# Kernel tuning notes

Hardware: AMD Instinct MI355X
Metric: run time of the kernel (lower is better)

Reference implementation:

```python
import jax, jax.numpy as jnp
import numpy as np

DIM = 768
NUM_HEADS = 12
HEAD_DIM = DIM // NUM_HEADS  # 64
HH = 48
WW = 48
REL_LEN = 2 * HH - 1  # 95
THETA = 10000.0


def _rope_freqs(dim, end_x, end_y, theta=THETA):
    # matches _compute_rope_frequencies: (end_x*end_y, dim//2) cos/sin tables
    freqs = 1.0 / theta ** (jnp.arange(0, dim, 4)[: dim // 4].astype(jnp.float32) / dim)
    t = jnp.arange(end_x * end_y, dtype=jnp.float32)
    t_x = t % end_x
    t_y = jnp.floor(t / end_x)
    f = jnp.concatenate([t_x[:, None] * freqs[None, :], t_y[:, None] * freqs[None, :]], axis=-1)
    return jnp.cos(f), jnp.sin(f)


def _rel_bias(size, rel_pos):
    # q_size == k_size == size, rel_pos already has length 2*size-1 -> pure gather
    coords = jnp.arange(size)[:, None] - jnp.arange(size)[None, :] + (size - 1)
    return rel_pos[coords]  # (size, size, C)


def setup_inputs() -> dict:
    key = jax.random.key(0)
    ks = jax.random.split(key, 6)
    x = jax.random.normal(ks[0], (1, HH, WW, DIM), dtype=jnp.float32)
    w_qkv = jax.random.normal(ks[1], (DIM, 3 * DIM), dtype=jnp.float32) * 0.02
    b_qkv = jnp.zeros((3 * DIM,), dtype=jnp.float32)
    w_proj = jax.random.normal(ks[2], (DIM, DIM), dtype=jnp.float32) * 0.02
    b_proj = jnp.zeros((DIM,), dtype=jnp.float32)
    rel_pos_h = jax.random.normal(ks[3], (REL_LEN, HEAD_DIM), dtype=jnp.float32) * 0.02
    rel_pos_w = jax.random.normal(ks[4], (REL_LEN, HEAD_DIM), dtype=jnp.float32) * 0.02
    return {"x": x, "w_qkv": w_qkv, "b_qkv": b_qkv, "w_proj": w_proj,
            "b_proj": b_proj, "rel_pos_h": rel_pos_h, "rel_pos_w": rel_pos_w}


def reference(x, w_qkv, b_qkv, w_proj, b_proj, rel_pos_h, rel_pos_w):
    B, H, W, dim = x.shape
    L = H * W
    nh, hd = NUM_HEADS, dim // NUM_HEADS
    scale = hd ** (-0.5)

    qkv = (x.reshape(B, L, dim) @ w_qkv + b_qkv).reshape(B, L, 3, nh, hd)
    qkv = qkv.transpose(2, 0, 3, 1, 4)  # (3, B, nh, L, hd)
    q, k, v = qkv[0], qkv[1], qkv[2]

    # inline RoPE (real-valued, pairwise rotation)
    cosf, sinf = _rope_freqs(hd, W, H)  # (L, hd//2)
    c = cosf[None, None]  # (1,1,L,hd//2)
    s = sinf[None, None]

    def rot(t):
        tr = t.reshape(B, nh, L, hd // 2, 2)
        t0, t1 = tr[..., 0], tr[..., 1]
        return jnp.stack([t0 * c - t1 * s, t0 * s + t1 * c], axis=-1).reshape(B, nh, L, hd)

    q = rot(q)
    k = rot(k)

    attn = jnp.einsum('bnqd,bnkd->bnqk', q, k) * scale  # (B, nh, L, L)

    # decomposed relative position bias
    bias_h = _rel_bias(H, rel_pos_h)  # (H, H, hd)
    bias_w = _rel_bias(W, rel_pos_w)  # (W, W, hd)
    q6 = q.reshape(B, nh, H, W, hd)
    rel_h = jnp.einsum('bnhwc,hkc->bnhwk', q6, bias_h)  # (B,nh,H,W,Hk)
    rel_w = jnp.einsum('bnhwc,wkc->bnhwk', q6, bias_w)  # (B,nh,H,W,Wk)
    attn = (attn.reshape(B, nh, H, W, H, W)
            + rel_h[..., :, None]   # broadcast over key-W
            + rel_w[..., None, :])  # broadcast over key-H
    attn = attn.reshape(B, nh, L, L)

    attn = jax.nn.softmax(attn, axis=-1)
    out = jnp.einsum('bnqk,bnkd->bnqd', attn, v)  # (B, nh, L, hd)
    out = out.transpose(0, 2, 1, 3).reshape(B, H, W, dim)
    return out @ w_proj + b_proj
```

## Files before the change

kernel.cpp:

```cpp
#include <hip/hip_runtime.h>
#include <hip/hip_bf16.h>


typedef short bf16x8 __attribute__((ext_vector_type(8)));
typedef float f32x4  __attribute__((ext_vector_type(4)));
typedef _Float16 f16x4 __attribute__((ext_vector_type(4)));

namespace {
constexpr int LTOK = 2304;
constexpr int DIMC = 768;
constexpr int NH   = 12;
constexpr int HD   = 64;
constexpr int WG   = 48;
constexpr int QKVN = 2304;
constexpr int EXT2 = 128;
constexpr int NSPLIT = 3;
constexpr int KPS  = LTOK / NSPLIT;
constexpr int NT   = KPS / 64;
constexpr int NQB2 = LTOK / 128;
constexpr float SCALE = 0.125f;
constexpr int NB_ROPE = (LTOK * 32) / 256;
constexpr int NB_CAST = (LTOK * DIMC / 8) / 256;
constexpr int NB_TQKV = (QKVN / 32) * (DIMC / 32);
constexpr int NB_TPRJ = (DIMC / 32) * (DIMC / 32);
}

__device__ __forceinline__ short f2b(float f) {
    __hip_bfloat16 h = __float2bfloat16(f);
    return *reinterpret_cast<short*>(&h);
}
__device__ __forceinline__ float b2f(short s) {
    return __uint_as_float(((unsigned)(unsigned short)s) << 16);
}
__device__ __forceinline__ void load16_to_lds(const short* g, short* l) {
    __builtin_amdgcn_global_load_lds(
        (__attribute__((address_space(1))) void*)g,
        (__attribute__((address_space(3))) void*)l,
        16, 0, 0);
}
__device__ __forceinline__ f16x4 nt_load_h4(const _Float16* p) {
    return __builtin_nontemporal_load((const f16x4*)p);
}

__global__ __launch_bounds__(256) void prep_kernel(
    const float* __restrict__ x, const float* __restrict__ w_qkv,
    const float* __restrict__ w_proj,
    float* __restrict__ cost, float* __restrict__ sint,
    short* __restrict__ xb, short* __restrict__ wqkvT, short* __restrict__ wprojT)
{
    __shared__ float ts[32][36];
    const int b = blockIdx.x;
    const int t = threadIdx.x;
    if (b < NB_ROPE) {
        int idx = b * 256 + t;
        int j = idx & 31;
        int l = idx >> 5;
        float tt = (j < 16) ? (float)(l % WG) : (float)(l / WG);
        int fi = j & 15;
        float freq = powf(10000.0f, -(float)fi / 16.0f);
        float ang = tt * freq;
        cost[idx] = cosf(ang);
        sint[idx] = sinf(ang);
    } else if (b < NB_ROPE + NB_CAST) {
        int i = (b - NB_ROPE) * 256 + t;
        float4 a = ((const float4*)x)[2 * i];
        float4 bb = ((const float4*)x)[2 * i + 1];
        bf16x8 o;
        o[0] = f2b(a.x); o[1] = f2b(a.y); o[2] = f2b(a.z); o[3] = f2b(a.w);
        o[4] = f2b(bb.x); o[5] = f2b(bb.y); o[6] = f2b(bb.z); o[7] = f2b(bb.w);
        ((bf16x8*)xb)[i] = o;
    } else {
        const float* in;
        short* out;
        int R, C, c0, r0;
        if (b < NB_ROPE + NB_CAST + NB_TQKV) {
            int flat = b - NB_ROPE - NB_CAST;
            in = w_qkv; out = wqkvT; R = DIMC; C = QKVN;
            c0 = (flat % (QKVN / 32)) * 32;
            r0 = (flat / (QKVN / 32)) * 32;
        } else {
            int flat = b - NB_ROPE - NB_CAST - NB_TQKV;
            in = w_proj; out = wprojT; R = DIMC; C = DIMC;
            c0 = (flat % (DIMC / 32)) * 32;
            r0 = (flat / (DIMC / 32)) * 32;
        }
        {
            int r = t >> 3, cb = (t & 7) * 4;
            float4 v = *(const float4*)&in[(size_t)(r0 + r) * C + c0 + cb];
            ts[r][cb] = v.x; ts[r][cb + 1] = v.y; ts[r][cb + 2] = v.z; ts[r][cb + 3] = v.w;
        }
        __syncthreads();
        {
            int oc = t >> 3, rb = (t & 7) * 4;
            short4 s;
            s.x = f2b(ts[rb][oc]);     s.y = f2b(ts[rb + 1][oc]);
            s.z = f2b(ts[rb + 2][oc]); s.w = f2b(ts[rb + 3][oc]);
            *(short4*)&out[(size_t)(c0 + oc) * R + r0 + rb] = s;
        }
    }
}

__global__ __launch_bounds__(256) void gemm_bf16_64x128_kernel(
    const short* __restrict__ A, const short* __restrict__ Bt,
    const float* __restrict__ bias, float* __restrict__ C,
    int M, int N, int K)
{
    __shared__ short As[64 * 64];
    __shared__ short Bs[128 * 64];
    const int tid = threadIdx.x;
    const int bm = blockIdx.y * 64, bn = blockIdx.x * 128;
    const int w = tid >> 6, l = tid & 63;
    const int lm = l & 15, lk = (l >> 4) * 8;

    f32x4 acc[4][2];
    const f32x4 zf = {0.f, 0.f, 0.f, 0.f};
    #pragma unroll
    for (int m = 0; m < 4; ++m)
        #pragma unroll
        for (int n = 0; n < 2; ++n) acc[m][n] = zf;

    for (int k0 = 0; k0 < K; k0 += 64) {
        __syncthreads();
        #pragma unroll
        for (int p = 0; p < 2; ++p) {
            int f = tid + p * 256;
            int row = f >> 3, c8 = (f & 7) * 8;
            load16_to_lds(&A[(size_t)(bm + row) * K + k0 + c8], &As[f * 8]);
        }
        #pragma unroll
        for (int p = 0; p < 4; ++p) {
            int f = tid + p * 256;
            int row = f >> 3, c8 = (f & 7) * 8;
            load16_to_lds(&Bt[(size_t)(bn + row) * K + k0 + c8], &Bs[f * 8]);
        }
        __syncthreads();
        #pragma unroll
        for (int kh = 0; kh < 2; ++kh) {
            bf16x8 a[4], b[2];
            #pragma unroll
            for (int m = 0; m < 4; ++m)
                a[m] = *(const bf16x8*)&As[(m * 16 + lm) * 64 + kh * 32 + lk];
            #pragma unroll
            for (int n = 0; n < 2; ++n)
                b[n] = *(const bf16x8*)&Bs[(w * 32 + n * 16 + lm) * 64 + kh * 32 + lk];
            #pragma unroll
            for (int m = 0; m < 4; ++m)
                #pragma unroll
                for (int n = 0; n < 2; ++n)
                    acc[m][n] = __builtin_amdgcn_mfma_f32_16x16x32_bf16(a[m], b[n], acc[m][n], 0, 0, 0);
        }
    }
    const int orow = (l >> 4) * 4;
    #pragma unroll
    for (int m = 0; m < 4; ++m) {
        #pragma unroll
        for (int n = 0; n < 2; ++n) {
            int col = bn + w * 32 + n * 16 + lm;
            float bv = bias[col];
            #pragma unroll
            for (int r = 0; r < 4; ++r) {
                int row = bm + m * 16 + orow + r;
                C[(size_t)row * N + col] = acc[m][n][r] + bv;
            }
        }
    }
}

__global__ __launch_bounds__(512) void gemm64_512_kernel(
    const short* __restrict__ A, const short* __restrict__ Bt,
    const float* __restrict__ bias, float* __restrict__ C,
    int M, int N, int K)
{
    __shared__ short As[64 * 64];
    __shared__ short Bs[64 * 64];
    const int tid = threadIdx.x;
    const int bm = blockIdx.y * 64, bn = blockIdx.x * 64;
    const int w = tid >> 6, l = tid & 63;
    const int wr = w >> 2;
    const int wc = w & 3;
    const int lm = l & 15, lk = (l >> 4) * 8;

    f32x4 acc[2][1];
    const f32x4 zf = {0.f, 0.f, 0.f, 0.f};
    acc[0][0] = zf; acc[1][0] = zf;

    for (int k0 = 0; k0 < K; k0 += 64) {
        __syncthreads();
        {
            int f = tid;
            int row = f >> 3, c8 = (f & 7) * 8;
            load16_to_lds(&A[(size_t)(bm + row) * K + k0 + c8], &As[f * 8]);
            load16_to_lds(&Bt[(size_t)(bn + row) * K + k0 + c8], &Bs[f * 8]);
        }
        __syncthreads();
        #pragma unroll
        for (int kh = 0; kh < 2; ++kh) {
            bf16x8 a[2], b;
            #pragma unroll
            for (int m = 0; m < 2; ++m)
                a[m] = *(const bf16x8*)&As[(wr * 32 + m * 16 + lm) * 64 + kh * 32 + lk];
            b = *(const bf16x8*)&Bs[(wc * 16 + lm) * 64 + kh * 32 + lk];
            #pragma unroll
            for (int m = 0; m < 2; ++m)
                acc[m][0] = __builtin_amdgcn_mfma_f32_16x16x32_bf16(a[m], b, acc[m][0], 0, 0, 0);
        }
    }
    const int orow = (l >> 4) * 4;
    #pragma unroll
    for (int m = 0; m < 2; ++m) {
        int col = bn + wc * 16 + lm;
        float bv = bias[col];
        #pragma unroll
        for (int r = 0; r < 4; ++r) {
            int row = bm + wr * 32 + m * 16 + orow + r;
            C[(size_t)row * N + col] = acc[m][0][r] + bv;
        }
    }
}

__global__ __launch_bounds__(256) void split_rope_relbias_kernel(
    const float* __restrict__ qkv_raw,
    const float* __restrict__ cost, const float* __restrict__ sint,
    const float* __restrict__ rel_pos_h, const float* __restrict__ rel_pos_w,
    short* __restrict__ q_ext, short* __restrict__ kb, short* __restrict__ vT,
    short* __restrict__ relh_g)
{
    __shared__ short vt_s[64][72];
    __shared__ float qf32[64][68];
    __shared__ float rph_st[49][68];
    __shared__ float rpw_st[95][68];
    __shared__ short outw[64][64];
    __shared__ short outh[64][48];

    const int h = blockIdx.y;
    const int l0 = blockIdx.x * 64;
    const int hmin = l0 / WG;
    const int t = threadIdx.x;
    const int tok = t >> 2, dq = (t & 3) * 16;
    const int l = l0 + tok;
    const float* row = qkv_raw + (size_t)l * QKVN + h * HD;

    bf16x8 qe[2], kv[2];
    #pragma unroll
    for (int i = 0; i < 16; i += 4) {
        int d = dq + i;
        float4 tq = *(const float4*)&row[d];
        float4 tk = *(const float4*)&row[DIMC + d];
        float4 tv = *(const float4*)&row[2 * DIMC + d];
        float2 c01 = *(const float2*)&cost[l * 32 + d / 2];
        float2 s01 = *(const float2*)&sint[l * 32 + d / 2];
        float q0 = tq.x * c01.x - tq.y * s01.x;
        float q1 = tq.x * s01.x + tq.y * c01.x;
        float q2 = tq.z * c01.y - tq.w * s01.y;
        float q3 = tq.z * s01.y + tq.w * c01.y;
        qe[i >> 3][(i & 7) + 0] = f2b(q0 * SCALE);
        qe[i >> 3][(i & 7) + 1] = f2b(q1 * SCALE);
        qe[i >> 3][(i & 7) + 2] = f2b(q2 * SCALE);
        qe[i >> 3][(i & 7) + 3] = f2b(q3 * SCALE);
        kv[i >> 3][(i & 7) + 0] = f2b(tk.x * c01.x - tk.y * s01.x);
        kv[i >> 3][(i & 7) + 1] = f2b(tk.x * s01.x + tk.y * c01.x);
        kv[i >> 3][(i & 7) + 2] = f2b(tk.z * c01.y - tk.w * s01.y);
        kv[i >> 3][(i & 7) + 3] = f2b(tk.z * s01.y + tk.w * c01.y);
        vt_s[d + 0][tok] = f2b(tv.x);
        vt_s[d + 1][tok] = f2b(tv.y);
        vt_s[d + 2][tok] = f2b(tv.z);
        vt_s[d + 3][tok] = f2b(tv.w);
    }
    size_t kbase = ((size_t)h * LTOK + l) * HD + dq;
    *(bf16x8*)&kb[kbase]     = kv[0];
    *(bf16x8*)&kb[kbase + 8] = kv[1];
    size_t ebase = ((size_t)h * LTOK + l) * EXT2 + dq;
    *(bf16x8*)&q_ext[ebase]     = qe[0];
    *(bf16x8*)&q_ext[ebase + 8] = qe[1];
    #pragma unroll
    for (int i = 0; i < 8; ++i) {
        qf32[tok][dq + i]     = b2f(qe[0][i]);
        qf32[tok][dq + 8 + i] = b2f(qe[1][i]);
    }
    {
        const bf16x8 z8 = {0, 0, 0, 0, 0, 0, 0, 0};
        ((bf16x8*)outw)[t] = z8;
        ((bf16x8*)outw)[t + 256] = z8;
    }
    __syncthreads();
    {
        const int drow = t >> 2, lq = (t & 3) * 16;
        bf16x8 v0 = *(bf16x8*)&vt_s[drow][lq];
        bf16x8 v1 = *(bf16x8*)&vt_s[drow][lq + 8];
        size_t vbase = ((size_t)h * HD + drow) * LTOK + l0 + lq;
        *(bf16x8*)&vT[vbase]     = v0;
        *(bf16x8*)&vT[vbase + 8] = v1;
    }
    for (int i = t; i < (49 + 95) * 16; i += 256) {
        int rr = i >> 4, c4 = (i & 15) * 4;
        if (rr < 49)
            *(float4*)&rph_st[rr][c4] = *(const float4*)&rel_pos_h[(size_t)(hmin + rr) * HD + c4];
        else
            *(float4*)&rpw_st[rr - 49][c4] = *(const float4*)&rel_pos_w[(size_t)(rr - 49) * HD + c4];
    }
    __syncthreads();
    {
        const int ti = t >> 2, sub = t & 3;
        const int ll = l0 + ti;
        const int hh = ll / WG, ww = ll % WG;
        const int hoff = hh - hmin;
        for (int ko = sub; ko < 96; ko += 4) {
            bool ish = ko < 48;
            int kk = ish ? ko : ko - 48;
            const float* br = ish ? &rph_st[hoff + 47 - kk][0] : &rpw_st[ww + 47 - kk][0];
            float s = 0.f;
            #pragma unroll
            for (int c = 0; c < HD; c += 4) {
                float4 a = *(const float4*)&qf32[ti][c];
                float4 b = *(const float4*)&br[c];
                s += a.x * b.x + a.y * b.y + a.z * b.z + a.w * b.w;
            }
            s *= 8.0f;
            if (ish) outh[ti][kk] = f2b(s);
            else     outw[ti][2 + kk] = f2b(s);
        }
    }
    __syncthreads();
    #pragma unroll
    for (int p = 0; p < 2; ++p) {
        int i = t + p * 256;
        int r2 = i >> 3, c8 = (i & 7) * 8;
        *(bf16x8*)&q_ext[((size_t)h * LTOK + l0 + r2) * EXT2 + 64 + c8] =
            *(const bf16x8*)&outw[r2][c8];
    }
    for (int i = t; i < 384; i += 256) {
        int r2 = i / 6, c8 = (i % 6) * 8;
        *(bf16x8*)&relh_g[((size_t)h * LTOK + l0 + r2) * WG + c8] =
            *(const bf16x8*)&outh[r2][c8];
    }
}

__global__ __launch_bounds__(256, 3) void attn_kernel(
    const short* __restrict__ q_ext, const short* __restrict__ kb,
    const short* __restrict__ vT, const short* __restrict__ relh_g,
    _Float16* __restrict__ o_part, float* __restrict__ lsum_g)
{
    __shared__ short ks[64][136];
    __shared__ short vs[64][72];
    __shared__ short rh[128][56];

    const int qblk = blockIdx.x;
    const int n = blockIdx.y;
    const int sp = blockIdx.z;
    const int q0 = qblk * 128;
    const int key_base = sp * KPS;
    const int tid = threadIdx.x;
    const int w = tid >> 6, l = tid & 63;
    const int lm = l & 15, g = l >> 4;
    const int lk = g * 8;

    const short* qeh = q_ext + (size_t)n * LTOK * EXT2;
    const short* kh  = kb + (size_t)n * LTOK * HD;
    const short* vh  = vT + (size_t)n * HD * LTOK;

    bf16x8 qf[2][4];
    #pragma unroll
    for (int t = 0; t < 2; ++t)
        #pragma unroll
        for (int kk = 0; kk < 4; ++kk)
            qf[t][kk] = *(const bf16x8*)&qeh[(size_t)(q0 + w * 32 + t * 16 + lm) * EXT2 + kk * 32 + lk];

    for (int i = tid; i < 128 * 6; i += 256) {
        int row = i / 6, c8 = (i % 6) * 8;
        *(bf16x8*)&rh[row][c8] =
            *(const bf16x8*)&relh_g[((size_t)n * LTOK + q0 + row) * WG + c8];
    }
    {
        const bf16x8 z8 = {0, 0, 0, 0, 0, 0, 0, 0};
        #pragma unroll
        for (int p = 0; p < 2; ++p) {
            int i = tid + p * 256;
            int row = i >> 3, c8 = (i & 7) * 8;
            *(bf16x8*)&ks[row][64 + c8] = z8;
        }
    }
    const short ONE = f2b(1.0f);
    int kap = 0, prev_wi = 66;
    if (tid < 64) {
        int f_ = tid >> 4, m_ = tid & 15;
        kap = 32 * (f_ >> 1) + 8 * (m_ >> 2) + 4 * (f_ & 1) + (m_ & 3);
        prev_wi = 66 + (key_base + kap) % WG;
    }

    bf16x8 kreg[2], vreg[2];
    #define ISSUE_LOADS(kt_)  do {                                              \
        const int key0_ = key_base + (kt_) * 64;                                \
        _Pragma("unroll")                                                       \
        for (int p = 0; p < 2; ++p) {                                           \
            int fl_ = tid + p * 256;                                            \
            int rho_ = fl_ >> 3, c8_ = (fl_ & 7) * 8;                           \
            int f_ = rho_ >> 4, m_ = rho_ & 15;                                 \
            int kap_ = 32 * (f_ >> 1) + 8 * (m_ >> 2) + 4 * (f_ & 1) + (m_ & 3);\
            kreg[p] = *(const bf16x8*)&kh[(size_t)(key0_ + kap_) * HD + c8_];   \
        }                                                                       \
        _Pragma("unroll")                                                       \
        for (int p = 0; p < 2; ++p) {                                           \
            int fl_ = tid + p * 256;                                            \
            int row_ = fl_ >> 3, c8_ = (fl_ & 7) * 8;                           \
            vreg[p] = *(const bf16x8*)&vh[(size_t)row_ * LTOK + key0_ + c8_];   \
        }                                                                       \
    } while (0)

    float lsum[2] = {0.f, 0.f};
    f32x4 oacc[2][4];
    const f32x4 zf = {0.f, 0.f, 0.f, 0.f};
    #pragma unroll
    for (int t = 0; t < 2; ++t)
        #pragma unroll
        for (int d = 0; d < 4; ++d) oacc[t][d] = zf;

    ISSUE_LOADS(0);

    for (int kt = 0; kt < NT; ++kt) {
        const int key0 = key_base + kt * 64;
        const int A = key0 / WG;
        const int T = WG * (A + 1);
        __syncthreads();
        #pragma unroll
        for (int p = 0; p < 2; ++p) {
            int fl = tid + p * 256;
            int rho = fl >> 3, c8 = (fl & 7) * 8;
            *(bf16x8*)&ks[rho][c8] = kreg[p];
        }
        #pragma unroll
        for (int p = 0; p < 2; ++p) {
            int fl = tid + p * 256;
            int row = fl >> 3, c8 = (fl & 7) * 8;
            *(bf16x8*)&vs[row][c8] = vreg[p];
        }
        if (tid < 64) {
            int key = key0 + kap;
            ks[tid][64] = (key < T) ? ONE : (short)0;
            ks[tid][65] = (key < T) ? (short)0 : ONE;
            ks[tid][prev_wi] = 0;
            int wcol = 66 + key % WG;
            ks[tid][wcol] = ONE;
            prev_wi = wcol;
        }
        if (kt + 1 < NT) { ISSUE_LOADS(kt + 1); }
        __builtin_amdgcn_sched_barrier(0);
        __syncthreads();

        if (g == 0) {
            #pragma unroll
            for (int t = 0; t < 2; ++t) {
                int row = w * 32 + t * 16 + lm;
                qf[t][2][0] = rh[row][A];
                qf[t][2][1] = rh[row][A + 1];
            }
        }

        f32x4 st[2][4];
        #pragma unroll
        for (int t = 0; t < 2; ++t)
            #pragma unroll
            for (int f = 0; f < 4; ++f) st[t][f] = zf;
        __builtin_amdgcn_s_setprio(1);
        #pragma unroll
        for (int f = 0; f < 4; ++f)
            #pragma unroll
            for (int kk = 0; kk < 4; ++kk) {
                bf16x8 kf = *(const bf16x8*)&ks[f * 16 + lm][kk * 32 + lk];
                st[0][f] = __builtin_amdgcn_mfma_f32_16x16x32_bf16(kf, qf[0][kk], st[0][f], 0, 0, 0);
                st[1][f] = __builtin_amdgcn_mfma_f32_16x16x32_bf16(kf, qf[1][kk], st[1][f], 0, 0, 0);
            }
        __builtin_amdgcn_s_setprio(0);
        bf16x8 pf[2][2];
        #pragma unroll
        for (int t = 0; t < 2; ++t)
            #pragma unroll
            for (int f = 0; f < 4; ++f)
                #pragma unroll
                for (int r = 0; r < 4; ++r) {
                    float p = __expf(st[t][f][r]);
                    lsum[t] += p;
                    pf[t][f >> 1][(f & 1) * 4 + r] = f2b(p);
                }
        __builtin_amdgcn_s_setprio(1);
        #pragma unroll
        for (int kk = 0; kk < 2; ++kk)
            #pragma unroll
            for (int d = 0; d < 4; ++d) {
                bf16x8 vf = *(const bf16x8*)&vs[d * 16 + lm][kk * 32 + lk];
                oacc[0][d] = __builtin_amdgcn_mfma_f32_16x16x32_bf16(pf[0][kk], vf, oacc[0][d], 0, 0, 0);
                oacc[1][d] = __builtin_amdgcn_mfma_f32_16x16x32_bf16(pf[1][kk], vf, oacc[1][d], 0, 0, 0);
            }
        __builtin_amdgcn_s_setprio(0);
    }
    #undef ISSUE_LOADS

    size_t pbase = (((size_t)n * NQB2 + qblk) * NSPLIT + sp) * (128 * 64);
    #pragma unroll
    for (int t = 0; t < 2; ++t)
        #pragma unroll
        for (int d = 0; d < 4; ++d) {
            f16x4 hv;
            #pragma unroll
            for (int r = 0; r < 4; ++r) hv[r] = (_Float16)oacc[t][d][r];
            __builtin_nontemporal_store(hv,
                (f16x4*)&o_part[pbase + (size_t)(((w * 2 + t) * 4 + d) * 256) + l * 4]);
        }
    size_t lb = (((size_t)n * NQB2 + qblk) * NSPLIT + sp) * 128;
    #pragma unroll
    for (int t = 0; t < 2; ++t) {
        float s = lsum[t];
        s += __shfl_xor(s, 16);
        s += __shfl_xor(s, 32);
        if (l < 16) lsum_g[lb + w * 32 + t * 16 + l] = s;
    }
}

__global__ __launch_bounds__(256) void combine_kernel(
    const _Float16* __restrict__ o_part, const float* __restrict__ lsum_g,
    short* __restrict__ o)
{
    __shared__ short ost[128][72];
    const int qblk = blockIdx.x, h = blockIdx.y;
    const int tid = threadIdx.x;
    const int w = tid >> 6, l = tid & 63;
    const int lm = l & 15, g = l >> 4;
    size_t sb = ((size_t)h * NQB2 + qblk) * NSPLIT;

    float inv[2][4];
    #pragma unroll
    for (int t = 0; t < 2; ++t)
        #pragma unroll
        for (int r = 0; r < 4; ++r) {
            int row = w * 32 + t * 16 + g * 4 + r;
            float ls = 0.f;
            #pragma unroll
            for (int s = 0; s < NSPLIT; ++s)
                ls += lsum_g[(sb + s) * 128 + row];
            inv[t][r] = 1.0f / ls;
        }
    #pragma unroll
    for (int t = 0; t < 2; ++t)
        #pragma unroll
        for (int d = 0; d < 4; ++d) {
            size_t off = (size_t)(((w * 2 + t) * 4 + d) * 256) + l * 4;
            float acc[4] = {0.f, 0.f, 0.f, 0.f};
            #pragma unroll
            for (int s = 0; s < NSPLIT; ++s) {
                f16x4 hv = nt_load_h4(&o_part[(sb + s) * 8192 + off]);
                #pragma unroll
                for (int r = 0; r < 4; ++r) acc[r] += (float)hv[r];
            }
            #pragma unroll
            for (int r = 0; r < 4; ++r)
                ost[w * 32 + t * 16 + g * 4 + r][d * 16 + lm] = f2b(acc[r] * inv[t][r]);
        }
    __syncthreads();
    const int row = tid >> 1, cb = (tid & 1) * 32;
    size_t ob = ((size_t)(qblk * 128 + row)) * DIMC + h * 64 + cb;
    #pragma unroll
    for (int v = 0; v < 4; ++v)
        *(bf16x8*)&o[ob + v * 8] = *(const bf16x8*)&ost[row][cb + v * 8];
}

extern "C" void kernel_launch(void* const* d_in, const int* in_sizes, int n_in,
                              void* d_out, int out_size, void* d_ws, size_t ws_size,
                              hipStream_t stream) {
    (void)in_sizes; (void)n_in; (void)out_size; (void)ws_size;
    const float* x         = (const float*)d_in[0];
    const float* w_qkv     = (const float*)d_in[1];
    const float* b_qkv     = (const float*)d_in[2];
    const float* w_proj    = (const float*)d_in[3];
    const float* b_proj    = (const float*)d_in[4];
    const float* rel_pos_h = (const float*)d_in[5];
    const float* rel_pos_w = (const float*)d_in[6];
    float* out = (float*)d_out;

    float* qkv_raw   = (float*)d_ws;
    short* xb        = (short*)(qkv_raw + (size_t)LTOK * QKVN);
    short* wqkvT     = xb + (size_t)LTOK * DIMC;
    float* cost      = (float*)(wqkvT + (size_t)QKVN * DIMC);
    float* sint      = cost + (size_t)LTOK * 32;
    _Float16* o_part = (_Float16*)qkv_raw;
    short* wprojT  = (short*)(sint + (size_t)LTOK * 32);
    short* q_ext   = wprojT + (size_t)DIMC * DIMC;
    short* kb      = q_ext + (size_t)NH * LTOK * EXT2;
    short* vTb     = kb + (size_t)NH * LTOK * HD;
    short* ob      = vTb + (size_t)NH * LTOK * HD;
    short* relh_g  = ob + (size_t)LTOK * DIMC;
    float* lsum_g  = (float*)(relh_g + (size_t)NH * LTOK * WG);

    prep_kernel<<<dim3(NB_ROPE + NB_CAST + NB_TQKV + NB_TPRJ), 256, 0, stream>>>(
        x, w_qkv, w_proj, cost, sint, xb, wqkvT, wprojT);

    gemm_bf16_64x128_kernel<<<dim3(QKVN / 128, LTOK / 64), 256, 0, stream>>>(
        xb, wqkvT, b_qkv, qkv_raw, LTOK, QKVN, DIMC);

    split_rope_relbias_kernel<<<dim3(LTOK / 64, NH), 256, 0, stream>>>(
        qkv_raw, cost, sint, rel_pos_h, rel_pos_w, q_ext, kb, vTb, relh_g);

    attn_kernel<<<dim3(NQB2, NH, NSPLIT), 256, 0, stream>>>(
        q_ext, kb, vTb, relh_g, o_part, lsum_g);

    combine_kernel<<<dim3(NQB2, NH), 256, 0, stream>>>(o_part, lsum_g, ob);

    gemm64_512_kernel<<<dim3(DIMC / 64, LTOK / 64), 512, 0, stream>>>(
        ob, wprojT, b_proj, out, LTOK, DIMC, DIMC);
}
```

Measured before the change: 97.30 us.

## Use 2-wave attention blocks with 64 query rows per wave; retile proj GEMM to 32x64

The attention kernel now runs 128 threads (2 waves) per block, and each wave handles 64 query rows instead of 32. Each K/V fragment read from LDS therefore feeds twice as many MFMAs, and the score computation is processed one key fragment at a time to limit live registers. The output projection GEMM moves from 64x64 tiles with 512 threads to 32x64 tiles with 256 threads, doubling the block count. The cost is higher register pressure in the attention kernel (larger oacc and qf arrays), fewer waves per CU for hiding latency, and more global-load work per thread.

Measured after the change: 116.1 us. 19.3% more time.

```diff
diff --git a/kernel.cpp b/kernel.cpp
--- a/kernel.cpp
+++ b/kernel.cpp
@@ -166,30 +166,32 @@
     }
 }
 
-__global__ __launch_bounds__(512) void gemm64_512_kernel(
+__global__ __launch_bounds__(256) void gemm32x64_kernel(
     const short* __restrict__ A, const short* __restrict__ Bt,
     const float* __restrict__ bias, float* __restrict__ C,
     int M, int N, int K)
 {
-    __shared__ short As[64 * 64];
+    __shared__ short As[32 * 64];
     __shared__ short Bs[64 * 64];
     const int tid = threadIdx.x;
-    const int bm = blockIdx.y * 64, bn = blockIdx.x * 64;
+    const int bm = blockIdx.y * 32, bn = blockIdx.x * 64;
     const int w = tid >> 6, l = tid & 63;
-    const int wr = w >> 2;
-    const int wc = w & 3;
     const int lm = l & 15, lk = (l >> 4) * 8;
 
-    f32x4 acc[2][1];
+    f32x4 acc[2];
     const f32x4 zf = {0.f, 0.f, 0.f, 0.f};
-    acc[0][0] = zf; acc[1][0] = zf;
+    acc[0] = zf; acc[1] = zf;
 
     for (int k0 = 0; k0 < K; k0 += 64) {
         __syncthreads();
         {
-            int f = tid;
+            int row = tid >> 3, c8 = (tid & 7) * 8;
+            load16_to_lds(&A[(size_t)(bm + row) * K + k0 + c8], &As[tid * 8]);
+        }
+        #pragma unroll
+        for (int p = 0; p < 2; ++p) {
+            int f = tid + p * 256;
             int row = f >> 3, c8 = (f & 7) * 8;
-            load16_to_lds(&A[(size_t)(bm + row) * K + k0 + c8], &As[f * 8]);
             load16_to_lds(&Bt[(size_t)(bn + row) * K + k0 + c8], &Bs[f * 8]);
         }
         __syncthreads();
@@ -198,22 +200,22 @@
             bf16x8 a[2], b;
             #pragma unroll
             for (int m = 0; m < 2; ++m)
-                a[m] = *(const bf16x8*)&As[(wr * 32 + m * 16 + lm) * 64 + kh * 32 + lk];
-            b = *(const bf16x8*)&Bs[(wc * 16 + lm) * 64 + kh * 32 + lk];
+                a[m] = *(const bf16x8*)&As[(m * 16 + lm) * 64 + kh * 32 + lk];
+            b = *(const bf16x8*)&Bs[(w * 16 + lm) * 64 + kh * 32 + lk];
             #pragma unroll
             for (int m = 0; m < 2; ++m)
-                acc[m][0] = __builtin_amdgcn_mfma_f32_16x16x32_bf16(a[m], b, acc[m][0], 0, 0, 0);
+                acc[m] = __builtin_amdgcn_mfma_f32_16x16x32_bf16(a[m], b, acc[m], 0, 0, 0);
         }
     }
     const int orow = (l >> 4) * 4;
     #pragma unroll
     for (int m = 0; m < 2; ++m) {
-        int col = bn + wc * 16 + lm;
+        int col = bn + w * 16 + lm;
         float bv = bias[col];
         #pragma unroll
         for (int r = 0; r < 4; ++r) {
-            int row = bm + wr * 32 + m * 16 + orow + r;
-            C[(size_t)row * N + col] = acc[m][0][r] + bv;
+            int row = bm + m * 16 + orow + r;
+            C[(size_t)row * N + col] = acc[m][r] + bv;
         }
     }
 }
@@ -335,7 +337,7 @@
     }
 }
 
-__global__ __launch_bounds__(256, 3) void attn_kernel(
+__global__ __launch_bounds__(128, 2) void attn_kernel(
     const short* __restrict__ q_ext, const short* __restrict__ kb,
     const short* __restrict__ vT, const short* __restrict__ relh_g,
     _Float16* __restrict__ o_part, float* __restrict__ lsum_g)
@@ -358,14 +360,14 @@
     const short* kh  = kb + (size_t)n * LTOK * HD;
     const short* vh  = vT + (size_t)n * HD * LTOK;
 
-    bf16x8 qf[2][4];
-    #pragma unroll
-    for (int t = 0; t < 2; ++t)
+    bf16x8 qf[4][4];
+    #pragma unroll
+    for (int t = 0; t < 4; ++t)
         #pragma unroll
         for (int kk = 0; kk < 4; ++kk)
-            qf[t][kk] = *(const bf16x8*)&qeh[(size_t)(q0 + w * 32 + t * 16 + lm) * EXT2 + kk * 32 + lk];
-
-    for (int i = tid; i < 128 * 6; i += 256) {
+            qf[t][kk] = *(const bf16x8*)&qeh[(size_t)(q0 + w * 64 + t * 16 + lm) * EXT2 + kk * 32 + lk];
+
+    for (int i = tid; i < 128 * 6; i += 128) {
         int row = i / 6, c8 = (i % 6) * 8;
         *(bf16x8*)&rh[row][c8] =
             *(const bf16x8*)&relh_g[((size_t)n * LTOK + q0 + row) * WG + c8];
@@ -373,8 +375,8 @@
     {
         const bf16x8 z8 = {0, 0, 0, 0, 0, 0, 0, 0};
         #pragma unroll
-        for (int p = 0; p < 2; ++p) {
-            int i = tid + p * 256;
+        for (int p = 0; p < 4; ++p) {
+            int i = tid + p * 128;
             int row = i >> 3, c8 = (i & 7) * 8;
             *(bf16x8*)&ks[row][64 + c8] = z8;
         }
@@ -387,30 +389,30 @@
         prev_wi = 66 + (key_base + kap) % WG;
     }
 
-    bf16x8 kreg[2], vreg[2];
+    bf16x8 kreg[4], vreg[4];
     #define ISSUE_LOADS(kt_)  do {                                              \
         const int key0_ = key_base + (kt_) * 64;                                \
         _Pragma("unroll")                                                       \
-        for (int p = 0; p < 2; ++p) {                                           \
-            int fl_ = tid + p * 256;                                            \
+        for (int p = 0; p < 4; ++p) {                                           \
+            int fl_ = tid + p * 128;                                            \
             int rho_ = fl_ >> 3, c8_ = (fl_ & 7) * 8;                           \
             int f_ = rho_ >> 4, m_ = rho_ & 15;                                 \
             int kap_ = 32 * (f_ >> 1) + 8 * (m_ >> 2) + 4 * (f_ & 1) + (m_ & 3);\
             kreg[p] = *(const bf16x8*)&kh[(size_t)(key0_ + kap_) * HD + c8_];   \
         }                                                                       \
         _Pragma("unroll")                                                       \
-        for (int p = 0; p < 2; ++p) {                                           \
-            int fl_ = tid + p * 256;                                            \
+        for (int p = 0; p < 4; ++p) {                                           \
+            int fl_ = tid + p * 128;                                            \
             int row_ = fl_ >> 3, c8_ = (fl_ & 7) * 8;                           \
             vreg[p] = *(const bf16x8*)&vh[(size_t)row_ * LTOK + key0_ + c8_];   \
         }                                                                       \
     } while (0)
 
-    float lsum[2] = {0.f, 0.f};
-    f32x4 oacc[2][4];
+    float lsum[4] = {0.f, 0.f, 0.f, 0.f};
+    f32x4 oacc[4][4];
     const f32x4 zf = {0.f, 0.f, 0.f, 0.f};
     #pragma unroll
-    for (int t = 0; t < 2; ++t)
+    for (int t = 0; t < 4; ++t)
         #pragma unroll
         for (int d = 0; d < 4; ++d) oacc[t][d] = zf;
 
@@ -422,14 +424,14 @@
         const int T = WG * (A + 1);
         __syncthreads();
         #pragma unroll
-        for (int p = 0; p < 2; ++p) {
-            int fl = tid + p * 256;
+        for (int p = 0; p < 4; ++p) {
+            int fl = tid + p * 128;
             int rho = fl >> 3, c8 = (fl & 7) * 8;
             *(bf16x8*)&ks[rho][c8] = kreg[p];
         }
         #pragma unroll
-        for (int p = 0; p < 2; ++p) {
-            int fl = tid + p * 256;
+        for (int p = 0; p < 4; ++p) {
+            int fl = tid + p * 128;
             int row = fl >> 3, c8 = (fl & 7) * 8;
             *(bf16x8*)&vs[row][c8] = vreg[p];
         }
@@ -448,47 +450,46 @@
 
         if (g == 0) {
             #pragma unroll
-            for (int t = 0; t < 2; ++t) {
-                int row = w * 32 + t * 16 + lm;
+            for (int t = 0; t < 4; ++t) {
+                int row = w * 64 + t * 16 + lm;
                 qf[t][2][0] = rh[row][A];
                 qf[t][2][1] = rh[row][A + 1];
             }
         }
 
-        f32x4 st[2][4];
-        #pragma unroll
-        for (int t = 0; t < 2; ++t)
-            #pragma unroll
-            for (int f = 0; f < 4; ++f) st[t][f] = zf;
-        __builtin_amdgcn_s_setprio(1);
-        #pragma unroll
-        for (int f = 0; f < 4; ++f)
+        bf16x8 pf[4][2];
+        #pragma unroll
+        for (int f = 0; f < 4; ++f) {
+            f32x4 stf[4];
+            #pragma unroll
+            for (int t = 0; t < 4; ++t) stf[t] = zf;
+            __builtin_amdgcn_s_setprio(1);
             #pragma unroll
             for (int kk = 0; kk < 4; ++kk) {
                 bf16x8 kf = *(const bf16x8*)&ks[f * 16 + lm][kk * 32 + lk];
-                st[0][f] = __builtin_amdgcn_mfma_f32_16x16x32_bf16(kf, qf[0][kk], st[0][f], 0, 0, 0);
-                st[1][f] = __builtin_amdgcn_mfma_f32_16x16x32_bf16(kf, qf[1][kk], st[1][f], 0, 0, 0);
+                #pragma unroll
+                for (int t = 0; t < 4; ++t)
+                    stf[t] = __builtin_amdgcn_mfma_f32_16x16x32_bf16(kf, qf[t][kk], stf[t], 0, 0, 0);
             }
-        __builtin_amdgcn_s_setprio(0);
-        bf16x8 pf[2][2];
-        #pragma unroll
-        for (int t = 0; t < 2; ++t)
-            #pragma unroll
-            for (int f = 0; f < 4; ++f)
+            __builtin_amdgcn_s_setprio(0);
+            #pragma unroll
+            for (int t = 0; t < 4; ++t)
                 #pragma unroll
                 for (int r = 0; r < 4; ++r) {
-                    float p = __expf(st[t][f][r]);
+                    float p = __expf(stf[t][r]);
                     lsum[t] += p;
                     pf[t][f >> 1][(f & 1) * 4 + r] = f2b(p);
                 }
+        }
         __builtin_amdgcn_s_setprio(1);
         #pragma unroll
         for (int kk = 0; kk < 2; ++kk)
             #pragma unroll
             for (int d = 0; d < 4; ++d) {
                 bf16x8 vf = *(const bf16x8*)&vs[d * 16 + lm][kk * 32 + lk];
-                oacc[0][d] = __builtin_amdgcn_mfma_f32_16x16x32_bf16(pf[0][kk], vf, oacc[0][d], 0, 0, 0);
-                oacc[1][d] = __builtin_amdgcn_mfma_f32_16x16x32_bf16(pf[1][kk], vf, oacc[1][d], 0, 0, 0);
+                #pragma unroll
+                for (int t = 0; t < 4; ++t)
+                    oacc[t][d] = __builtin_amdgcn_mfma_f32_16x16x32_bf16(pf[t][kk], vf, oacc[t][d], 0, 0, 0);
             }
         __builtin_amdgcn_s_setprio(0);
     }
@@ -496,22 +497,22 @@
 
     size_t pbase = (((size_t)n * NQB2 + qblk) * NSPLIT + sp) * (128 * 64);
     #pragma unroll
-    for (int t = 0; t < 2; ++t)
+    for (int t = 0; t < 4; ++t)
         #pragma unroll
         for (int d = 0; d < 4; ++d) {
             f16x4 hv;
             #pragma unroll
             for (int r = 0; r < 4; ++r) hv[r] = (_Float16)oacc[t][d][r];
             __builtin_nontemporal_store(hv,
-                (f16x4*)&o_part[pbase + (size_t)(((w * 2 + t) * 4 + d) * 256) + l * 4]);
+                (f16x4*)&o_part[pbase + (size_t)(((w * 4 + t) * 4 + d) * 256) + l * 4]);
         }
     size_t lb = (((size_t)n * NQB2 + qblk) * NSPLIT + sp) * 128;
     #pragma unroll
-    for (int t = 0; t < 2; ++t) {
+    for (int t = 0; t < 4; ++t) {
         float s = lsum[t];
         s += __shfl_xor(s, 16);
         s += __shfl_xor(s, 32);
-        if (l < 16) lsum_g[lb + w * 32 + t * 16 + l] = s;
+        if (l < 16) lsum_g[lb + w * 64 + t * 16 + l] = s;
     }
 }
 
@@ -598,11 +599,11 @@
     split_rope_relbias_kernel<<<dim3(LTOK / 64, NH), 256, 0, stream>>>(
         qkv_raw, cost, sint, rel_pos_h, rel_pos_w, q_ext, kb, vTb, relh_g);
 
-    attn_kernel<<<dim3(NQB2, NH, NSPLIT), 256, 0, stream>>>(
+    attn_kernel<<<dim3(NQB2, NH, NSPLIT), 128, 0, stream>>>(
         q_ext, kb, vTb, relh_g, o_part, lsum_g);
 
     combine_kernel<<<dim3(NQB2, NH), 256, 0, stream>>>(o_part, lsum_g, ob);
 
-    gemm64_512_kernel<<<dim3(DIMC / 64, LTOK / 64), 512, 0, stream>>>(
+    gemm32x64_kernel<<<dim3(DIMC / 64, LTOK / 32), 256, 0, stream>>>(
         ob, wprojT, b_proj, out, LTOK, DIMC, DIMC);
 }
```
